# Kernel tuning notes

Measured on AMD Instinct MI355X. Metric: run time of the kernel, lower is better.

Reference implementation:

```python
import jax, jax.numpy as jnp
import numpy as np

F_DIM = 64
GRID_CYL = (512, 48)   # (grid0=azimuth, grid1=z)
CYL_RANGE = (-3.14159265, -2.0, 3.14159265, 4.0)
CYL_VS = ((CYL_RANGE[2] - CYL_RANGE[0]) / GRID_CYL[0], (CYL_RANGE[3] - CYL_RANGE[1]) / GRID_CYL[1])
PC_RANGE = (0.0, -40.0, -3.0, 70.4, 40.0, 1.0)
BEV_VS = (0.32, 0.32)
GRID_BEV = (220, 250)  # (grid0=x, grid1=y)
BEV_SCALE_XY = GRID_BEV[0] * GRID_BEV[1]
BEV_SCALE_Y = GRID_BEV[1]
CYL_SCALE_XY = GRID_CYL[0] * GRID_CYL[1]
CYL_SCALE_Y = GRID_CYL[1]
BN_EPS = 1e-3


def _bn_relu(x, g, b):
    # train-mode BatchNorm1d over point axis; x: [N, C]
    m = x.mean(0)
    v = jnp.mean((x - m) ** 2, 0)
    return jax.nn.relu((x - m) * jax.lax.rsqrt(v + BN_EPS) * g + b)


def setup_inputs():
    rng = np.random.default_rng(0)
    B, NP = 4, 50000
    N = B * NP
    bidx = np.repeat(np.arange(B), NP).astype(np.float32)
    x = rng.uniform(0.5, 70.0, N).astype(np.float32)
    y = rng.uniform(-39.9, 39.9, N).astype(np.float32)
    z = rng.uniform(-2.9, 0.9, N).astype(np.float32)
    inten = rng.uniform(0.0, 1.0, N).astype(np.float32)
    points = np.stack([bidx, x, y, z, inten], 1)
    rho = np.sqrt(x * x + y * y)
    phi = np.arctan2(y, x)
    points_cyl = np.stack([phi, z, rho], 1).astype(np.float32)
    cyl_idxs = np.stack([(phi - CYL_RANGE[0]) / CYL_VS[0], (z - CYL_RANGE[1]) / CYL_VS[1]], 1)
    cyl_idxs = np.minimum(np.maximum(cyl_idxs, 0.0), np.array(GRID_CYL) - 1e-3).astype(np.float32)
    bev_idxs = np.stack([(x - PC_RANGE[0]) / BEV_VS[0], (y - PC_RANGE[1]) / BEV_VS[1]], 1)
    bev_idxs = np.minimum(np.maximum(bev_idxs, 0.0), np.array(GRID_BEV) - 1e-3).astype(np.float32)
    bev_merge = bidx.astype(np.int64) * BEV_SCALE_XY + np.floor(bev_idxs[:, 0]).astype(np.int64) * BEV_SCALE_Y + np.floor(bev_idxs[:, 1]).astype(np.int64)
    bev_unq, bev_inv = np.unique(bev_merge, return_inverse=True)
    cyl_merge = bidx.astype(np.int64) * CYL_SCALE_XY + np.floor(cyl_idxs[:, 0]).astype(np.int64) * CYL_SCALE_Y + np.floor(cyl_idxs[:, 1]).astype(np.int64)
    cyl_unq, cyl_inv = np.unique(cyl_merge, return_inverse=True)

    def lin(o, i):
        return (rng.standard_normal((o, i)) / np.sqrt(i)).astype(np.float32)

    w1 = lin(F_DIM, 16)
    w2 = lin(2 * F_DIM, F_DIM)
    w3 = lin(F_DIM, 2 * F_DIM)
    wc = (rng.standard_normal((F_DIM, F_DIM, 3, 3)) / np.sqrt(F_DIM * 9)).astype(np.float32)

    def bn(c):
        return (1.0 + 0.1 * rng.standard_normal(c)).astype(np.float32), (0.1 * rng.standard_normal(c)).astype(np.float32)

    g1, b1 = bn(F_DIM)
    g2, b2 = bn(2 * F_DIM)
    gc, bc = bn(F_DIM)
    g3, b3 = bn(F_DIM)
    return {
        'points': jnp.asarray(points), 'points_cyl': jnp.asarray(points_cyl),
        'cyl_idxs': jnp.asarray(cyl_idxs), 'bev_idxs': jnp.asarray(bev_idxs),
        'w1': jnp.asarray(w1), 'g1': jnp.asarray(g1), 'b1': jnp.asarray(b1),
        'w2': jnp.asarray(w2), 'g2': jnp.asarray(g2), 'b2': jnp.asarray(b2),
        'wc': jnp.asarray(wc), 'gc': jnp.asarray(gc), 'bc': jnp.asarray(bc),
        'w3': jnp.asarray(w3), 'g3': jnp.asarray(g3), 'b3': jnp.asarray(b3),
        'bev_unq_inv': jnp.asarray(bev_inv.astype(np.int32)),
        'bev_unq_coords': jnp.asarray(bev_unq.astype(np.int32)),
        'cyl_unq_inv': jnp.asarray(cyl_inv.astype(np.int32)),
        'cyl_unq_coords': jnp.asarray(cyl_unq.astype(np.int32)),
        'batch_size': B,
    }


def reference(points, points_cyl, cyl_idxs, bev_idxs, w1, g1, b1, w2, g2, b2, wc, gc, bc, w3, g3, b3, bev_unq_inv, bev_unq_coords, cyl_unq_inv, cyl_unq_coords, batch_size):
    N = points.shape[0]
    xyz = points[:, 1:4]
    feat = points[:, 4:]
    pbatch = points[:, 0].astype(jnp.int32)
    bev_c = jnp.floor(bev_idxs)
    cyl_c = jnp.floor(cyl_idxs)
    Nb = bev_unq_coords.shape[0]
    Nc = cyl_unq_coords.shape[0]
    ones = jnp.ones((N,), points.dtype)
    # scatter_mean + gather centering / clustering features
    cnt_b = jax.ops.segment_sum(ones, bev_unq_inv, Nb)
    bev_mean = jax.ops.segment_sum(xyz, bev_unq_inv, Nb) / cnt_b[:, None]
    bev_f_cluster = (xyz - bev_mean[bev_unq_inv])[:, :2]
    bev_f_center = xyz[:, :2] - ((bev_c + 0.5) * jnp.array(BEV_VS, points.dtype) + jnp.array(PC_RANGE[:2], points.dtype))
    cnt_c = jax.ops.segment_sum(ones, cyl_unq_inv, Nc)
    cyl_mean = jax.ops.segment_sum(points_cyl, cyl_unq_inv, Nc) / cnt_c[:, None]
    cyl_f_cluster = (points_cyl - cyl_mean[cyl_unq_inv])[:, :2]
    cyl_f_center = points_cyl[:, :2] - ((cyl_c + 0.5) * jnp.array(CYL_VS, points.dtype) + jnp.array(CYL_RANGE[:2], points.dtype))
    dist = jnp.sqrt(jnp.sum(xyz ** 2, 1, keepdims=True))
    mvf_in = jnp.concatenate([xyz, points_cyl, bev_f_center, cyl_f_center, bev_f_cluster, cyl_f_cluster, dist, feat], 1)  # [N,16]
    # input_transform: two 1x1 Conv1d (= matmul) + BN + ReLU
    h = _bn_relu(mvf_in @ w1.T, g1, b1)   # [N,64]
    h2 = _bn_relu(h @ w2.T, g2, b2)       # [N,128]
    pt_fea_cyl, pointwise = h2[:, :F_DIM], h2[:, F_DIM:]
    # cyl scatter_max -> dense range-view grid
    cyl_max = jax.ops.segment_max(pt_fea_cyl, cyl_unq_inv, Nc)  # [Nc,64]
    cb = cyl_unq_coords // CYL_SCALE_XY
    rem = cyl_unq_coords % CYL_SCALE_XY
    cx = rem // CYL_SCALE_Y
    cy = rem % CYL_SCALE_Y
    dense = jnp.zeros((batch_size, CYL_SCALE_XY, F_DIM), cyl_max.dtype)
    dense = dense.at[cb, cy * GRID_CYL[0] + cx].set(cyl_max)
    img = dense.reshape(batch_size, GRID_CYL[1], GRID_CYL[0], F_DIM).transpose(0, 3, 2, 1)  # NCHW, H=grid0, W=grid1
    # cyl_net proxy: Conv2d 3x3 + BN + ReLU
    img = jax.lax.conv_general_dilated(img, wc, (1, 1), 'SAME', dimension_numbers=('NCHW', 'OIHW', 'NCHW'))
    m = img.mean((0, 2, 3), keepdims=True)
    v = jnp.mean((img - m) ** 2, (0, 2, 3), keepdims=True)
    img = jax.nn.relu((img - m) * jax.lax.rsqrt(v + BN_EPS) * gc[None, :, None, None] + bc[None, :, None, None])
    im = img.transpose(0, 2, 3, 1)  # [B, grid0, grid1, F]
    # bilinear interpolation of per-point cyl features
    yq, xq = cyl_idxs[:, 0], cyl_idxs[:, 1]
    x0 = jnp.clip(jnp.floor(xq).astype(jnp.int32), 0, GRID_CYL[1] - 1)
    x1 = jnp.clip(jnp.floor(xq).astype(jnp.int32) + 1, 0, GRID_CYL[1] - 1)
    y0 = jnp.clip(jnp.floor(yq).astype(jnp.int32), 0, GRID_CYL[0] - 1)
    y1 = jnp.clip(jnp.floor(yq).astype(jnp.int32) + 1, 0, GRID_CYL[0] - 1)
    Ia = im[pbatch, y0, x0]
    Ib = im[pbatch, y1, x0]
    Ic = im[pbatch, y0, x1]
    Id = im[pbatch, y1, x1]
    x0f, x1f = x0.astype(xq.dtype), x1.astype(xq.dtype)
    y0f, y1f = y0.astype(yq.dtype), y1.astype(yq.dtype)
    wa = (x1f - xq) * (y1f - yq)
    wb_ = (x1f - xq) * (yq - y0f)
    wc_ = (xq - x0f) * (y1f - yq)
    wd = (xq - x0f) * (yq - y0f)
    point_cyl = Ia * wa[:, None] + Ib * wb_[:, None] + Ic * wc_[:, None] + Id * wd[:, None]  # [N,64]
    # mvf pointnet + bev scatter_max
    mvf2 = jnp.concatenate([pointwise, point_cyl], 1)  # [N,128]
    mvf_fea = _bn_relu(mvf2 @ w3.T, g3, b3)            # [N,64]
    bev_max = jax.ops.segment_max(mvf_fea, bev_unq_inv, Nb)  # [Nb,64] pillar features
    vb = bev_unq_coords // BEV_SCALE_XY
    vx = (bev_unq_coords % BEV_SCALE_XY) // BEV_SCALE_Y
    vy = bev_unq_coords % BEV_SCALE_Y
    voxel_coords = jnp.stack([vb, jnp.zeros_like(vb), vy, vx], 1)
    return mvf_fea, bev_max, voxel_coords
```

## Files before the change

kernel.cpp:

```cpp
#include <hip/hip_runtime.h>
#include <math.h>

#define BN_EPS 1e-3f

static constexpr float CR0 = -3.14159265f;
static constexpr float CR1 = -2.0f;
static constexpr float CVS0 = (float)((3.14159265 * 2.0) / 512.0);
static constexpr float CVS1 = (float)(6.0 / 48.0);
#define BEV_SXY (220 * 250)
#define BEV_SY 250

typedef __attribute__((ext_vector_type(8))) __bf16 bf16x8_t;
typedef __attribute__((ext_vector_type(4))) float f32x4_t;

union ABu { uint4 q; unsigned short us[8]; bf16x8_t bf; };

__device__ __forceinline__ float bnr(float x, float a, float b) {
    float v = fmaf(x, a, b);
    return v > 0.f ? v : 0.f;
}
__device__ __forceinline__ float bf2f(unsigned short u) {
    return __uint_as_float(((unsigned)u) << 16);
}
__device__ __forceinline__ unsigned short f2bf(float f) {
    unsigned u = __float_as_uint(f);
    u += 0x7FFFu + ((u >> 16) & 1u);
    return (unsigned short)(u >> 16);
}
__device__ __forceinline__ void bn_ab(const float* st, const float* g, const float* b,
                                      int C, int ch, float invn, float& a, float& bb) {
    float m = st[ch] * invn;
    float var = st[C + ch] * invn - m * m;
    a = g[ch] * rsqrtf(var + BN_EPS);
    bb = b[ch] - m * a;
}

__device__ __forceinline__ unsigned fkey(float f) {
    unsigned u = __float_as_uint(f);
    return (u & 0x80000000u) ? ~u : (u | 0x80000000u);
}
__device__ __forceinline__ float dec_key(unsigned k, float a, float b) {
    if (k == 0u) return 0.f;
    unsigned u = (k & 0x80000000u) ? (k ^ 0x80000000u) : ~k;
    float v = fmaf(__uint_as_float(u), a, b);
    return v > 0.f ? v : 0.f;
}

__global__ void k_scatter_sums(const float* __restrict__ pts, const float* __restrict__ pcyl,
                               const int* __restrict__ binv, const int* __restrict__ cinv,
                               const float* __restrict__ wc, unsigned short* __restrict__ wctb,
                               unsigned long long* __restrict__ bacc,
                               unsigned long long* __restrict__ cacc,
                               int N, int Nb, int Nc) {
    int p = blockIdx.x * blockDim.x + threadIdx.x;
    if (p < 9 * 4096) {
        int j = p & 7, oc = (p >> 3) & 63, quad = (p >> 9) & 3, kc = (p >> 11) & 1, tap = p >> 12;
        int ic = kc * 32 + quad * 8 + j;
        wctb[p] = f2bf(wc[((oc * 64 + ic) * 3 + tap / 3) * 3 + tap % 3]);
    }
    if (p >= N) return;
    float x = pts[p * 5 + 1], y = pts[p * 5 + 2];
    float ph = pcyl[p * 3 + 0], z = pcyl[p * 3 + 1];
    int bi = binv[p], ci = cinv[p];
    unsigned long long xa = (1ull << 44) + (unsigned long long)(x * 1048576.0f + 0.5f);
    unsigned long long ya = (unsigned long long)((y + 40.0f) * 16777216.0f + 0.5f);
    unsigned long long pa = (1ull << 44) + (unsigned long long)((ph + 3.14159265f) * 16777216.0f + 0.5f);
    unsigned long long za = (unsigned long long)((z + 3.0f) * 16777216.0f + 0.5f);
    atomicAdd(&bacc[2 * (long)bi], xa);
    atomicAdd(&bacc[2 * (long)bi + 1], ya);
    atomicAdd(&cacc[2 * (long)ci], pa);
    atomicAdd(&cacc[2 * (long)ci + 1], za);
}

__global__ __launch_bounds__(256) void k_feat_gemm1(const float* __restrict__ pts,
        const float* __restrict__ pcyl, const float* __restrict__ cylidx,
        const float* __restrict__ bevidx, const int* __restrict__ binv,
        const int* __restrict__ cinv, const unsigned long long* __restrict__ bacc,
        const unsigned long long* __restrict__ cacc, const float* __restrict__ w1,
        unsigned short* __restrict__ h1b, int N, int Nb, int Nc) {
    __shared__ float w1s[1024];
    __shared__ unsigned int tbuf[32 * 260];
    int t = threadIdx.x;
    for (int i = t; i < 1024; i += 256) w1s[i] = w1[i];
    __syncthreads();
    int p = blockIdx.x * 256 + t;
    int pc = min(p, N - 1);
    float x = pts[pc * 5 + 1], y = pts[pc * 5 + 2], z = pts[pc * 5 + 3], inten = pts[pc * 5 + 4];
    float ph = pcyl[pc * 3 + 0], zc = pcyl[pc * 3 + 1], rho = pcyl[pc * 3 + 2];
    float ci0 = cylidx[pc * 2 + 0], ci1 = cylidx[pc * 2 + 1];
    float bi0 = bevidx[pc * 2 + 0], bi1 = bevidx[pc * 2 + 1];
    float bc0 = floorf(bi0), bc1 = floorf(bi1);
    float cc0 = floorf(ci0), cc1 = floorf(ci1);
    int bv = binv[pc], cv = cinv[pc];
    const unsigned long long MASK44 = (1ull << 44) - 1ull;
    unsigned long long A = bacc[2 * (long)bv], Bq = bacc[2 * (long)bv + 1];
    float bcnt = (float)(A >> 44);
    float rb = 1.0f / bcnt;
    float bmx = (float)(A & MASK44) * (1.0f / 1048576.0f) * rb;
    float bmy = (float)Bq * (1.0f / 16777216.0f) * rb - 40.0f;
    unsigned long long Cq = cacc[2 * (long)cv], Dq = cacc[2 * (long)cv + 1];
    float ccnt = (float)(Cq >> 44);
    float rc = 1.0f / ccnt;
    float cmp = (float)(Cq & MASK44) * (1.0f / 16777216.0f) * rc - 3.14159265f;
    float cmz = (float)Dq * (1.0f / 16777216.0f) * rc - 3.0f;
    float f[16];
    f[0] = x; f[1] = y; f[2] = z;
    f[3] = ph; f[4] = zc; f[5] = rho;
    f[6] = x - ((bc0 + 0.5f) * 0.32f + 0.0f);
    f[7] = y - ((bc1 + 0.5f) * 0.32f + (-40.0f));
    f[8] = ph - ((cc0 + 0.5f) * CVS0 + CR0);
    f[9] = zc - ((cc1 + 0.5f) * CVS1 + CR1);
    f[10] = x - bmx; f[11] = y - bmy;
    f[12] = ph - cmp; f[13] = zc - cmz;
    f[14] = sqrtf(x * x + y * y + z * z);
    f[15] = inten;
    for (int c2 = 0; c2 < 32; c2++) {
        float s0 = 0.f, s1 = 0.f;
        const float* w0 = &w1s[(2 * c2) * 16];
        const float* w1p = &w1s[(2 * c2 + 1) * 16];
#pragma unroll
        for (int k = 0; k < 16; k++) {
            s0 = fmaf(f[k], w0[k], s0);
            s1 = fmaf(f[k], w1p[k], s1);
        }
        tbuf[c2 * 260 + t] = (unsigned)f2bf(s0) | ((unsigned)f2bf(s1) << 16);
    }
    __syncthreads();
#pragma unroll
    for (int r = 0; r < 4; r++) {
        int cid = t + 256 * r;
        int pp = cid >> 2;
        int gp = blockIdx.x * 256 + pp;
        if (gp < N) {
            int c2b = (cid & 3) * 8;
            uint4 A2, Bv;
            A2.x = tbuf[(c2b + 0) * 260 + pp];
            A2.y = tbuf[(c2b + 1) * 260 + pp];
            A2.z = tbuf[(c2b + 2) * 260 + pp];
            A2.w = tbuf[(c2b + 3) * 260 + pp];
            Bv.x = tbuf[(c2b + 4) * 260 + pp];
            Bv.y = tbuf[(c2b + 5) * 260 + pp];
            Bv.z = tbuf[(c2b + 6) * 260 + pp];
            Bv.w = tbuf[(c2b + 7) * 260 + pp];
            uint4* dst = (uint4*)(h1b + (long)gp * 64 + (cid & 3) * 16);
            dst[0] = A2;
            dst[1] = Bv;
        }
    }
}

__global__ __launch_bounds__(256) void k_stats_v(const unsigned short* __restrict__ buf,
        long T, int C, float* __restrict__ out) {
    int t = threadIdx.x;
    long base = ((long)blockIdx.x * 256 + t) * 8;
    long stride = (long)gridDim.x * 2048;
    float s[8], q[8];
#pragma unroll
    for (int j = 0; j < 8; j++) { s[j] = 0.f; q[j] = 0.f; }
    for (long i = base; i < T; i += stride) {
        ABu u;
        u.q = *(const uint4*)(buf + i);
#pragma unroll
        for (int j = 0; j < 8; j++) {
            float v = bf2f(u.us[j]);
            s[j] += v;
            q[j] = fmaf(v, v, q[j]);
        }
    }
    __shared__ float ls[2048], lq[2048];
#pragma unroll
    for (int j = 0; j < 8; j++) { ls[t * 8 + j] = s[j]; lq[t * 8 + j] = q[j]; }
    __syncthreads();
    if (t < C) {
        int g = t >> 3, j = t & 7;
        int step = C >> 3;
        float ss = 0.f, qq = 0.f;
        for (int tid = g; tid < 256; tid += step) {
            ss += ls[tid * 8 + j];
            qq += lq[tid * 8 + j];
        }
        atomicAdd(&out[t], ss);
        atomicAdd(&out[C + t], qq);
    }
}

__global__ __launch_bounds__(256, 2) void k_gemm2_mfma(const unsigned short* __restrict__ h1b,
        const float* __restrict__ w2, const float* __restrict__ st1,
        const float* __restrict__ g1, const float* __restrict__ b1g, float invn,
        const float* __restrict__ pts, const float* __restrict__ cylidx,
        const float* __restrict__ g2full, unsigned int* __restrict__ gridk,
        unsigned short* __restrict__ h2b, int N) {
    int lane = threadIdx.x & 63;
    int c = lane & 15, quad = lane >> 4;
    int wid = (blockIdx.x * 256 + threadIdx.x) >> 6;
    int nw = gridDim.x * 4;
    bf16x8_t Bf[8][2];
#pragma unroll
    for (int tt = 0; tt < 8; tt++)
#pragma unroll
        for (int kc = 0; kc < 2; kc++) {
            const float* wr = w2 + (tt * 16 + c) * 64 + kc * 32 + quad * 8;
            float4 w0 = *(const float4*)wr;
            float4 w1 = *(const float4*)(wr + 4);
            ABu tmp;
            tmp.us[0] = f2bf(w0.x); tmp.us[1] = f2bf(w0.y);
            tmp.us[2] = f2bf(w0.z); tmp.us[3] = f2bf(w0.w);
            tmp.us[4] = f2bf(w1.x); tmp.us[5] = f2bf(w1.y);
            tmp.us[6] = f2bf(w1.z); tmp.us[7] = f2bf(w1.w);
            Bf[tt][kc] = tmp.bf;
        }
    float a1[16], b1[16];
#pragma unroll
    for (int kc = 0; kc < 2; kc++)
#pragma unroll
        for (int j = 0; j < 8; j++) {
            int ch = kc * 32 + quad * 8 + j;
            bn_ab(st1, g1, b1g, 64, ch, invn, a1[kc * 8 + j], b1[kc * 8 + j]);
        }
    unsigned sx[4];
#pragma unroll
    for (int tt = 0; tt < 4; tt++)
        sx[tt] = (g2full[tt * 16 + c] < 0.f) ? 0x80000000u : 0u;
    int ntiles = (N + 15) >> 4;
    for (int tile = wid; tile < ntiles; tile += nw) {
        int p0 = tile * 16;
        int pa = min(p0 + c, N - 1);
        int bsc = (int)pts[pa * 5];
        int ccx = (int)floorf(cylidx[pa * 2]);
        int ccy = (int)floorf(cylidx[pa * 2 + 1]);
        int cellbase = (((bsc * 512 + ccx) * 48) + ccy) * 64;
        bf16x8_t Af[2];
#pragma unroll
        for (int kc = 0; kc < 2; kc++) {
            ABu u;
            u.q = *(const uint4*)(h1b + (long)pa * 64 + kc * 32 + quad * 8);
            ABu o;
#pragma unroll
            for (int j = 0; j < 8; j++)
                o.us[j] = f2bf(bnr(bf2f(u.us[j]), a1[kc * 8 + j], b1[kc * 8 + j]));
            Af[kc] = o.bf;
        }
        f32x4_t acc[8];
#pragma unroll
        for (int tt = 0; tt < 8; tt++) acc[tt] = (f32x4_t){0.f, 0.f, 0.f, 0.f};
#pragma unroll
        for (int tt = 0; tt < 8; tt++) {
            acc[tt] = __builtin_amdgcn_mfma_f32_16x16x32_bf16(Af[0], Bf[tt][0], acc[tt], 0, 0, 0);
            acc[tt] = __builtin_amdgcn_mfma_f32_16x16x32_bf16(Af[1], Bf[tt][1], acc[tt], 0, 0, 0);
        }
#pragma unroll
        for (int r = 0; r < 4; r++) {
            int cb_r = __shfl(cellbase, quad * 4 + r);
            int pr = p0 + quad * 4 + r;
            bool ok = pr < N;
#pragma unroll
            for (int tt = 0; tt < 8; tt++) {
                unsigned short hv = f2bf(acc[tt][r]);
                if (ok) {
                    h2b[(long)pr * 128 + tt * 16 + c] = hv;
                    if (tt < 4) {
                        float xr = bf2f(hv);
                        unsigned key = fkey(__uint_as_float(__float_as_uint(xr) ^ sx[tt]));
                        atomicMax(&gridk[cb_r + tt * 16 + c], key);
                    }
                }
            }
        }
    }
}

__global__ __launch_bounds__(768) void k_conv_lds(const unsigned int* __restrict__ gridk,
        const unsigned short* __restrict__ wctb, unsigned short* __restrict__ cb,
        const float* __restrict__ st2, const float* __restrict__ g2,
        const float* __restrict__ b2g, float invn) {
    __shared__ unsigned short in_s[4 * 50 * 64];
    __shared__ unsigned short ob_s[2 * 48 * 64];
    __shared__ float as_[64], bs_[64];
    int t = threadIdx.x;
    int lane = t & 63, wv = t >> 6;
    int n = lane & 15, quad = lane >> 4;
    int seg = wv >> 2, tt = wv & 3;
    int blk = blockIdx.x;
    int b = blk >> 8, r0 = (blk & 255) * 2;
    if (t < 64) {
        float av, bv;
        bn_ab(st2, g2, b2g, 128, t, invn, av, bv);
        as_[t] = fabsf(av);
        bs_[t] = bv;
    }
    bf16x8_t Bf[9][2];
    const unsigned short* wb = wctb + quad * 512 + (tt * 16 + n) * 8;
#pragma unroll
    for (int tap = 0; tap < 9; tap++)
#pragma unroll
        for (int kc = 0; kc < 2; kc++) {
            ABu u;
            u.q = *(const uint4*)(wb + (tap * 2 + kc) * 2048);
            Bf[tap][kc] = u.bf;
        }
    __syncthreads();
    for (int c = t; c < 1600; c += 768) {
        int row4 = c / 400;
        int rem = c % 400;
        int px = rem >> 3, ch8 = rem & 7;
        int gr = r0 + row4 - 1, gw = px - 1;
        ABu o;
        if (gr >= 0 && gr < 512 && gw >= 0 && gw < 48) {
            const unsigned int* src = gridk + (((long)b * 512 + gr) * 48 + gw) * 64 + ch8 * 8;
            uint4 k0 = *(const uint4*)src;
            uint4 k1 = *(const uint4*)(src + 4);
            const float* ap = &as_[ch8 * 8];
            const float* bp = &bs_[ch8 * 8];
            o.us[0] = f2bf(dec_key(k0.x, ap[0], bp[0]));
            o.us[1] = f2bf(dec_key(k0.y, ap[1], bp[1]));
            o.us[2] = f2bf(dec_key(k0.z, ap[2], bp[2]));
            o.us[3] = f2bf(dec_key(k0.w, ap[3], bp[3]));
            o.us[4] = f2bf(dec_key(k1.x, ap[4], bp[4]));
            o.us[5] = f2bf(dec_key(k1.y, ap[5], bp[5]));
            o.us[6] = f2bf(dec_key(k1.z, ap[6], bp[6]));
            o.us[7] = f2bf(dec_key(k1.w, ap[7], bp[7]));
        } else {
            o.q = make_uint4(0, 0, 0, 0);
        }
        *(uint4*)&in_s[(row4 * 50 + px) * 64 + ((ch8 ^ (px & 7)) << 3)] = o.q;
    }
    __syncthreads();
    for (int rr = 0; rr < 2; rr++) {
        f32x4_t acc0 = (f32x4_t){0.f, 0.f, 0.f, 0.f};
        f32x4_t acc1 = (f32x4_t){0.f, 0.f, 0.f, 0.f};
#pragma unroll
        for (int tap = 0; tap < 9; tap++) {
            int row4 = tap / 3 + rr;
            int lpx = seg * 16 + n + tap % 3;
            const unsigned short* base = &in_s[(row4 * 50 + lpx) * 64];
            ABu a0, a1;
            a0.q = *(const uint4*)(base + ((quad ^ (lpx & 7)) << 3));
            a1.q = *(const uint4*)(base + (((4 + quad) ^ (lpx & 7)) << 3));
            acc0 = __builtin_amdgcn_mfma_f32_16x16x32_bf16(a0.bf, Bf[tap][0], acc0, 0, 0, 0);
            acc1 = __builtin_amdgcn_mfma_f32_16x16x32_bf16(a1.bf, Bf[tap][1], acc1, 0, 0, 0);
        }
#pragma unroll
        for (int r2 = 0; r2 < 4; r2++) {
            int px = seg * 16 + quad * 4 + r2;
            ob_s[(rr * 48 + px) * 64 + tt * 16 + n] = f2bf(acc0[r2] + acc1[r2]);
        }
    }
    __syncthreads();
    unsigned short* dst = cb + ((long)b * 512 + r0) * 48 * 64;
    *(uint4*)(dst + t * 8) = *(const uint4*)(ob_s + t * 8);
}

__global__ __launch_bounds__(256, 2) void k_gather3_mfma(const unsigned short* __restrict__ h2b,
        const unsigned short* __restrict__ convb, const float* __restrict__ st2,
        const float* __restrict__ g2, const float* __restrict__ b2g,
        const float* __restrict__ stC, const float* __restrict__ gc,
        const float* __restrict__ bcg, float invn, float invnC,
        const float* __restrict__ cylidx, const float* __restrict__ pts,
        const float* __restrict__ w3, unsigned short* __restrict__ h3b, int N) {
    int lane = threadIdx.x & 63;
    int c = lane & 15, quad = lane >> 4;
    int wid = (blockIdx.x * 256 + threadIdx.x) >> 6;
    int nw = gridDim.x * 4;
    bf16x8_t Bf[4][4];
#pragma unroll
    for (int tt = 0; tt < 4; tt++)
#pragma unroll
        for (int kc = 0; kc < 4; kc++) {
            const float* wr = w3 + (tt * 16 + c) * 128 + kc * 32 + quad * 8;
            float4 w0 = *(const float4*)wr;
            float4 w1 = *(const float4*)(wr + 4);
            ABu tmp;
            tmp.us[0] = f2bf(w0.x); tmp.us[1] = f2bf(w0.y);
            tmp.us[2] = f2bf(w0.z); tmp.us[3] = f2bf(w0.w);
            tmp.us[4] = f2bf(w1.x); tmp.us[5] = f2bf(w1.y);
            tmp.us[6] = f2bf(w1.z); tmp.us[7] = f2bf(w1.w);
            Bf[tt][kc] = tmp.bf;
        }
    float a2[16], b2[16], aC[16], bC[16];
#pragma unroll
    for (int kc = 0; kc < 2; kc++)
#pragma unroll
        for (int j = 0; j < 8; j++) {
            int kk = kc * 32 + quad * 8 + j;
            bn_ab(st2, g2, b2g, 128, 64 + kk, invn, a2[kc * 8 + j], b2[kc * 8 + j]);
            bn_ab(stC, gc, bcg, 64, kk, invnC, aC[kc * 8 + j], bC[kc * 8 + j]);
        }
    int ntiles = (N + 15) >> 4;
    for (int tile = wid; tile < ntiles; tile += nw) {
        int p0 = tile * 16;
        int p = min(p0 + c, N - 1);
        float yq = cylidx[p * 2], xq = cylidx[p * 2 + 1];
        int b = (int)pts[p * 5];
        int xf = (int)floorf(xq), yf = (int)floorf(yq);
        int x0 = min(max(xf, 0), 47);
        int x1 = min(max(xf + 1, 0), 47);
        int y0 = min(max(yf, 0), 511);
        int y1 = min(max(yf + 1, 0), 511);
        float x0f = (float)x0, x1f = (float)x1, y0f = (float)y0, y1f = (float)y1;
        float wa = (x1f - xq) * (y1f - yq);
        float wb = (x1f - xq) * (yq - y0f);
        float wc2 = (xq - x0f) * (y1f - yq);
        float wd = (xq - x0f) * (yq - y0f);
        const unsigned short* Ia = convb + (((long)b * 512 + y0) * 48 + x0) * 64;
        const unsigned short* Ib = convb + (((long)b * 512 + y1) * 48 + x0) * 64;
        const unsigned short* Ic = convb + (((long)b * 512 + y0) * 48 + x1) * 64;
        const unsigned short* Id = convb + (((long)b * 512 + y1) * 48 + x1) * 64;
        bf16x8_t Af[4];
#pragma unroll
        for (int kc = 0; kc < 2; kc++) {
            ABu u;
            u.q = *(const uint4*)(h2b + (long)p * 128 + 64 + kc * 32 + quad * 8);
            ABu o;
#pragma unroll
            for (int j = 0; j < 8; j++)
                o.us[j] = f2bf(bnr(bf2f(u.us[j]), a2[kc * 8 + j], b2[kc * 8 + j]));
            Af[kc] = o.bf;
        }
#pragma unroll
        for (int kc = 0; kc < 2; kc++) {
            int cbo = kc * 32 + quad * 8;
            ABu ua, ub, uc, ud;
            ua.q = *(const uint4*)(Ia + cbo);
            ub.q = *(const uint4*)(Ib + cbo);
            uc.q = *(const uint4*)(Ic + cbo);
            ud.q = *(const uint4*)(Id + cbo);
            ABu o;
#pragma unroll
            for (int j = 0; j < 8; j++) {
                float aa = aC[kc * 8 + j], bbv = bC[kc * 8 + j];
                float v = wa * bnr(bf2f(ua.us[j]), aa, bbv) + wb * bnr(bf2f(ub.us[j]), aa, bbv)
                        + wc2 * bnr(bf2f(uc.us[j]), aa, bbv) + wd * bnr(bf2f(ud.us[j]), aa, bbv);
                o.us[j] = f2bf(v);
            }
            Af[2 + kc] = o.bf;
        }
        f32x4_t acc[4];
#pragma unroll
        for (int tt = 0; tt < 4; tt++) acc[tt] = (f32x4_t){0.f, 0.f, 0.f, 0.f};
#pragma unroll
        for (int tt = 0; tt < 4; tt++)
#pragma unroll
            for (int kc = 0; kc < 4; kc++)
                acc[tt] = __builtin_amdgcn_mfma_f32_16x16x32_bf16(Af[kc], Bf[tt][kc], acc[tt], 0, 0, 0);
#pragma unroll
        for (int tt = 0; tt < 4; tt++)
#pragma unroll
            for (int r = 0; r < 4; r++) {
                int pr = p0 + quad * 4 + r;
                if (pr < N) h3b[(long)pr * 64 + tt * 16 + c] = f2bf(acc[tt][r]);
            }
    }
}

__global__ __launch_bounds__(256) void k_out_tile3(const unsigned short* __restrict__ h3b,
        const float* __restrict__ st3, const float* __restrict__ g3,
        const float* __restrict__ b3g, float invn, const int* __restrict__ binv,
        float* __restrict__ out_fea, unsigned int* __restrict__ out_bev,
        const int* __restrict__ bcoords, float* __restrict__ out_vc, int Nb, int N) {
    int t = threadIdx.x, lane = t & 63, w = t >> 6;
    long gid = (long)blockIdx.x * 256 + t;
    if (gid < Nb) {
        int cc = bcoords[gid];
        int vb = cc / BEV_SXY;
        int rem = cc % BEV_SXY;
        int vx = rem / BEV_SY;
        int vy = rem % BEV_SY;
        out_vc[gid * 4 + 0] = (float)vb;
        out_vc[gid * 4 + 1] = 0.f;
        out_vc[gid * 4 + 2] = (float)vy;
        out_vc[gid * 4 + 3] = (float)vx;
    }
    int p = blockIdx.x * 4 + w;
    if (p >= N) return;
    float a, bb;
    bn_ab(st3, g3, b3g, 64, lane, invn, a, bb);
    float v = bnr(bf2f(h3b[(long)p * 64 + lane]), a, bb);
    out_fea[(long)p * 64 + lane] = v;
    int bi = binv[p];
    if (v > 0.f) {
        unsigned uv = __float_as_uint(v);
        unsigned* cell = out_bev + (long)bi * 64;
        unsigned cur = cell[lane];
        if (uv > cur) atomicMax(&cell[lane], uv);
    }
}

extern "C" void kernel_launch(void* const* d_in, const int* in_sizes, int n_in,
                              void* d_out, int out_size, void* d_ws, size_t ws_size,
                              hipStream_t stream) {
    const float* pts = (const float*)d_in[0];
    const float* pcyl = (const float*)d_in[1];
    const float* cylidx = (const float*)d_in[2];
    const float* bevidx = (const float*)d_in[3];
    const float* w1 = (const float*)d_in[4];
    const float* g1 = (const float*)d_in[5];
    const float* b1 = (const float*)d_in[6];
    const float* w2 = (const float*)d_in[7];
    const float* g2 = (const float*)d_in[8];
    const float* b2 = (const float*)d_in[9];
    const float* wc = (const float*)d_in[10];
    const float* gc = (const float*)d_in[11];
    const float* bc = (const float*)d_in[12];
    const float* w3 = (const float*)d_in[13];
    const float* g3 = (const float*)d_in[14];
    const float* b3 = (const float*)d_in[15];
    const int* binv = (const int*)d_in[16];
    const int* bcoords = (const int*)d_in[17];
    const int* cinv = (const int*)d_in[18];
    const int* ccoords = (const int*)d_in[19];
    int N = in_sizes[0] / 5;
    int Nb = in_sizes[17];
    int Nc = in_sizes[19];
    const int B = 4;
    const long GRIDSZ = (long)B * 512 * 48 * 64;
    float invN = 1.0f / (float)N;
    float invC = 1.0f / (float)(B * 512 * 48);

    char* wsb = (char*)d_ws;
    unsigned short* wctb = (unsigned short*)wsb;
    unsigned short* h2b = (unsigned short*)(wsb + 73728);
    unsigned short* h13b = (unsigned short*)(wsb + 73728 + 256L * N);
    unsigned int* gridk = (unsigned int*)(wsb + 73728 + 384L * N);
    unsigned short* convb = (unsigned short*)(gridk + GRIDSZ);
    unsigned long long* bacc = (unsigned long long*)(convb + GRIDSZ);
    unsigned long long* cacc = bacc + 2L * Nb;
    float* stats = (float*)(cacc + 2L * Nc);
    float* st1 = stats, *st2 = stats + 128, *st3 = stats + 384, *stC = stats + 512;

    float* out_fea = (float*)d_out;
    unsigned int* out_bev = (unsigned int*)((float*)d_out + (long)N * 64);
    float* out_vc = (float*)d_out + (long)N * 64 + (long)Nb * 64;

    hipMemsetAsync(gridk, 0, (size_t)GRIDSZ * 4, stream);
    hipMemsetAsync(bacc, 0, (size_t)((2L * Nb + 2L * Nc) * 8 + 768 * 4), stream);
    hipMemsetAsync(out_bev, 0, (size_t)Nb * 64 * 4, stream);

    int nb256 = (N + 255) / 256;
    k_scatter_sums<<<nb256, 256, 0, stream>>>(pts, pcyl, binv, cinv, wc, wctb, bacc, cacc, N, Nb, Nc);
    k_feat_gemm1<<<nb256, 256, 0, stream>>>(pts, pcyl, cylidx, bevidx, binv, cinv, bacc, cacc, w1, h13b, N, Nb, Nc);
    k_stats_v<<<512, 256, 0, stream>>>(h13b, 64L * N, 64, st1);
    k_gemm2_mfma<<<512, 256, 0, stream>>>(h13b, w2, st1, g1, b1, invN, pts, cylidx, g2, gridk, h2b, N);
    k_stats_v<<<512, 256, 0, stream>>>(h2b, 128L * N, 128, st2);
    k_conv_lds<<<1024, 768, 0, stream>>>(gridk, wctb, convb, st2, g2, b2, invN);
    k_stats_v<<<512, 256, 0, stream>>>(convb, GRIDSZ, 64, stC);
    k_gather3_mfma<<<512, 256, 0, stream>>>(h2b, convb, st2, g2, b2, stC, gc, bc, invN, invC, cylidx, pts, w3, h13b, N);
    k_stats_v<<<512, 256, 0, stream>>>(h13b, 64L * N, 64, st3);
    k_out_tile3<<<(N + 3) / 4, 256, 0, stream>>>(h13b, st3, g3, b3, invN, binv, out_fea, out_bev, bcoords, out_vc, Nb, N);
}
```

Before: 444.1 us.

## Fuse BatchNorm statistics into producer kernels and halve the h2 buffer

Removes the four standalone k_stats_v passes. Each producer kernel (gemm1, gemm2, conv, gather3) now accumulates per-channel sum and sum-of-squares of its bf16 outputs in registers or LDS, reduces across the wave, and adds them atomically into the stats buffer. gemm2 no longer writes the first 64 channels of h2 to memory, since they only feed the grid atomicMax, so h2 becomes 64 channels wide and gather3 reads it that way. Grid sizes for gemm2 and gather3 are doubled. The cost is more float atomics on the stats arrays and a non-deterministic summation order.

```diff
diff --git a/kernel.cpp b/kernel.cpp
--- a/kernel.cpp
+++ b/kernel.cpp
@@ -77,7 +77,8 @@
         const float* __restrict__ bevidx, const int* __restrict__ binv,
         const int* __restrict__ cinv, const unsigned long long* __restrict__ bacc,
         const unsigned long long* __restrict__ cacc, const float* __restrict__ w1,
-        unsigned short* __restrict__ h1b, int N, int Nb, int Nc) {
+        unsigned short* __restrict__ h1b, float* __restrict__ st1o,
+        int N, int Nb, int Nc) {
     __shared__ float w1s[1024];
     __shared__ unsigned int tbuf[32 * 260];
     int t = threadIdx.x;
@@ -147,40 +148,30 @@
             dst[1] = Bv;
         }
     }
-}
-
-__global__ __launch_bounds__(256) void k_stats_v(const unsigned short* __restrict__ buf,
-        long T, int C, float* __restrict__ out) {
-    int t = threadIdx.x;
-    long base = ((long)blockIdx.x * 256 + t) * 8;
-    long stride = (long)gridDim.x * 2048;
-    float s[8], q[8];
-#pragma unroll
-    for (int j = 0; j < 8; j++) { s[j] = 0.f; q[j] = 0.f; }
-    for (long i = base; i < T; i += stride) {
-        ABu u;
-        u.q = *(const uint4*)(buf + i);
-#pragma unroll
-        for (int j = 0; j < 8; j++) {
-            float v = bf2f(u.us[j]);
-            s[j] += v;
-            q[j] = fmaf(v, v, q[j]);
-        }
-    }
-    __shared__ float ls[2048], lq[2048];
-#pragma unroll
-    for (int j = 0; j < 8; j++) { ls[t * 8 + j] = s[j]; lq[t * 8 + j] = q[j]; }
-    __syncthreads();
-    if (t < C) {
-        int g = t >> 3, j = t & 7;
-        int step = C >> 3;
+    {
+        int ch = t & 63, grp = t >> 6;
+        int c2 = ch >> 1, sh = (ch & 1) << 4;
+        int nval = min(256, N - blockIdx.x * 256);
         float ss = 0.f, qq = 0.f;
-        for (int tid = g; tid < 256; tid += step) {
-            ss += ls[tid * 8 + j];
-            qq += lq[tid * 8 + j];
-        }
-        atomicAdd(&out[t], ss);
-        atomicAdd(&out[C + t], qq);
+        for (int i = 0; i < 64; i++) {
+            int pp = grp * 64 + i;
+            if (pp < nval) {
+                unsigned uw = tbuf[c2 * 260 + pp];
+                float v = bf2f((unsigned short)(uw >> sh));
+                ss += v;
+                qq = fmaf(v, v, qq);
+            }
+        }
+        __syncthreads();
+        w1s[t] = ss;
+        w1s[256 + t] = qq;
+        __syncthreads();
+        if (t < 64) {
+            float S = w1s[t] + w1s[64 + t] + w1s[128 + t] + w1s[192 + t];
+            float Q = w1s[256 + t] + w1s[320 + t] + w1s[384 + t] + w1s[448 + t];
+            atomicAdd(&st1o[t], S);
+            atomicAdd(&st1o[64 + t], Q);
+        }
     }
 }
 
@@ -189,7 +180,7 @@
         const float* __restrict__ g1, const float* __restrict__ b1g, float invn,
         const float* __restrict__ pts, const float* __restrict__ cylidx,
         const float* __restrict__ g2full, unsigned int* __restrict__ gridk,
-        unsigned short* __restrict__ h2b, int N) {
+        unsigned short* __restrict__ h2b, float* __restrict__ st2o, int N) {
     int lane = threadIdx.x & 63;
     int c = lane & 15, quad = lane >> 4;
     int wid = (blockIdx.x * 256 + threadIdx.x) >> 6;
@@ -221,6 +212,9 @@
 #pragma unroll
     for (int tt = 0; tt < 4; tt++)
         sx[tt] = (g2full[tt * 16 + c] < 0.f) ? 0x80000000u : 0u;
+    float s8[8], q8[8];
+#pragma unroll
+    for (int tt = 0; tt < 8; tt++) { s8[tt] = 0.f; q8[tt] = 0.f; }
     int ntiles = (N + 15) >> 4;
     for (int tile = wid; tile < ntiles; tile += nw) {
         int p0 = tile * 16;
@@ -257,22 +251,35 @@
             for (int tt = 0; tt < 8; tt++) {
                 unsigned short hv = f2bf(acc[tt][r]);
                 if (ok) {
-                    h2b[(long)pr * 128 + tt * 16 + c] = hv;
+                    float xr = bf2f(hv);
+                    s8[tt] += xr;
+                    q8[tt] = fmaf(xr, xr, q8[tt]);
                     if (tt < 4) {
-                        float xr = bf2f(hv);
                         unsigned key = fkey(__uint_as_float(__float_as_uint(xr) ^ sx[tt]));
                         atomicMax(&gridk[cb_r + tt * 16 + c], key);
+                    } else {
+                        h2b[(long)pr * 64 + (tt - 4) * 16 + c] = hv;
                     }
                 }
             }
         }
     }
+#pragma unroll
+    for (int tt = 0; tt < 8; tt++) {
+        float ss = s8[tt], qq = q8[tt];
+        ss += __shfl_xor(ss, 16); ss += __shfl_xor(ss, 32);
+        qq += __shfl_xor(qq, 16); qq += __shfl_xor(qq, 32);
+        if (quad == 0) {
+            atomicAdd(&st2o[tt * 16 + c], ss);
+            atomicAdd(&st2o[128 + tt * 16 + c], qq);
+        }
+    }
 }
 
 __global__ __launch_bounds__(768) void k_conv_lds(const unsigned int* __restrict__ gridk,
         const unsigned short* __restrict__ wctb, unsigned short* __restrict__ cb,
         const float* __restrict__ st2, const float* __restrict__ g2,
-        const float* __restrict__ b2g, float invn) {
+        const float* __restrict__ b2g, float invn, float* __restrict__ stCo) {
     __shared__ unsigned short in_s[4 * 50 * 64];
     __shared__ unsigned short ob_s[2 * 48 * 64];
     __shared__ float as_[64], bs_[64];
@@ -325,6 +332,7 @@
         *(uint4*)&in_s[(row4 * 50 + px) * 64 + ((ch8 ^ (px & 7)) << 3)] = o.q;
     }
     __syncthreads();
+    float sC = 0.f, qC = 0.f;
     for (int rr = 0; rr < 2; rr++) {
         f32x4_t acc0 = (f32x4_t){0.f, 0.f, 0.f, 0.f};
         f32x4_t acc1 = (f32x4_t){0.f, 0.f, 0.f, 0.f};
@@ -342,8 +350,18 @@
 #pragma unroll
         for (int r2 = 0; r2 < 4; r2++) {
             int px = seg * 16 + quad * 4 + r2;
-            ob_s[(rr * 48 + px) * 64 + tt * 16 + n] = f2bf(acc0[r2] + acc1[r2]);
-        }
+            unsigned short hv = f2bf(acc0[r2] + acc1[r2]);
+            ob_s[(rr * 48 + px) * 64 + tt * 16 + n] = hv;
+            float xr = bf2f(hv);
+            sC += xr;
+            qC = fmaf(xr, xr, qC);
+        }
+    }
+    sC += __shfl_xor(sC, 16); sC += __shfl_xor(sC, 32);
+    qC += __shfl_xor(qC, 16); qC += __shfl_xor(qC, 32);
+    if (quad == 0) {
+        atomicAdd(&stCo[tt * 16 + n], sC);
+        atomicAdd(&stCo[64 + tt * 16 + n], qC);
     }
     __syncthreads();
     unsigned short* dst = cb + ((long)b * 512 + r0) * 48 * 64;
@@ -356,7 +374,8 @@
         const float* __restrict__ stC, const float* __restrict__ gc,
         const float* __restrict__ bcg, float invn, float invnC,
         const float* __restrict__ cylidx, const float* __restrict__ pts,
-        const float* __restrict__ w3, unsigned short* __restrict__ h3b, int N) {
+        const float* __restrict__ w3, unsigned short* __restrict__ h3b,
+        float* __restrict__ st3o, int N) {
     int lane = threadIdx.x & 63;
     int c = lane & 15, quad = lane >> 4;
     int wid = (blockIdx.x * 256 + threadIdx.x) >> 6;
@@ -385,6 +404,9 @@
             bn_ab(st2, g2, b2g, 128, 64 + kk, invn, a2[kc * 8 + j], b2[kc * 8 + j]);
             bn_ab(stC, gc, bcg, 64, kk, invnC, aC[kc * 8 + j], bC[kc * 8 + j]);
         }
+    float s4[4], q4[4];
+#pragma unroll
+    for (int tt = 0; tt < 4; tt++) { s4[tt] = 0.f; q4[tt] = 0.f; }
     int ntiles = (N + 15) >> 4;
     for (int tile = wid; tile < ntiles; tile += nw) {
         int p0 = tile * 16;
@@ -409,7 +431,7 @@
 #pragma unroll
         for (int kc = 0; kc < 2; kc++) {
             ABu u;
-            u.q = *(const uint4*)(h2b + (long)p * 128 + 64 + kc * 32 + quad * 8);
+            u.q = *(const uint4*)(h2b + (long)p * 64 + kc * 32 + quad * 8);
             ABu o;
 #pragma unroll
             for (int j = 0; j < 8; j++)
@@ -447,8 +469,24 @@
 #pragma unroll
             for (int r = 0; r < 4; r++) {
                 int pr = p0 + quad * 4 + r;
-                if (pr < N) h3b[(long)pr * 64 + tt * 16 + c] = f2bf(acc[tt][r]);
+                if (pr < N) {
+                    unsigned short hv = f2bf(acc[tt][r]);
+                    h3b[(long)pr * 64 + tt * 16 + c] = hv;
+                    float xr = bf2f(hv);
+                    s4[tt] += xr;
+                    q4[tt] = fmaf(xr, xr, q4[tt]);
+                }
             }
+    }
+#pragma unroll
+    for (int tt = 0; tt < 4; tt++) {
+        float ss = s4[tt], qq = q4[tt];
+        ss += __shfl_xor(ss, 16); ss += __shfl_xor(ss, 32);
+        qq += __shfl_xor(qq, 16); qq += __shfl_xor(qq, 32);
+        if (quad == 0) {
+            atomicAdd(&st3o[tt * 16 + c], ss);
+            atomicAdd(&st3o[64 + tt * 16 + c], qq);
+        }
     }
 }
 
@@ -519,8 +557,8 @@
     char* wsb = (char*)d_ws;
     unsigned short* wctb = (unsigned short*)wsb;
     unsigned short* h2b = (unsigned short*)(wsb + 73728);
-    unsigned short* h13b = (unsigned short*)(wsb + 73728 + 256L * N);
-    unsigned int* gridk = (unsigned int*)(wsb + 73728 + 384L * N);
+    unsigned short* h13b = (unsigned short*)(wsb + 73728 + 128L * N);
+    unsigned int* gridk = (unsigned int*)(wsb + 73728 + 256L * N);
     unsigned short* convb = (unsigned short*)(gridk + GRIDSZ);
     unsigned long long* bacc = (unsigned long long*)(convb + GRIDSZ);
     unsigned long long* cacc = bacc + 2L * Nb;
@@ -537,13 +575,9 @@
 
     int nb256 = (N + 255) / 256;
     k_scatter_sums<<<nb256, 256, 0, stream>>>(pts, pcyl, binv, cinv, wc, wctb, bacc, cacc, N, Nb, Nc);
-    k_feat_gemm1<<<nb256, 256, 0, stream>>>(pts, pcyl, cylidx, bevidx, binv, cinv, bacc, cacc, w1, h13b, N, Nb, Nc);
-    k_stats_v<<<512, 256, 0, stream>>>(h13b, 64L * N, 64, st1);
-    k_gemm2_mfma<<<512, 256, 0, stream>>>(h13b, w2, st1, g1, b1, invN, pts, cylidx, g2, gridk, h2b, N);
-    k_stats_v<<<512, 256, 0, stream>>>(h2b, 128L * N, 128, st2);
-    k_conv_lds<<<1024, 768, 0, stream>>>(gridk, wctb, convb, st2, g2, b2, invN);
-    k_stats_v<<<512, 256, 0, stream>>>(convb, GRIDSZ, 64, stC);
-    k_gather3_mfma<<<512, 256, 0, stream>>>(h2b, convb, st2, g2, b2, stC, gc, bc, invN, invC, cylidx, pts, w3, h13b, N);
-    k_stats_v<<<512, 256, 0, stream>>>(h13b, 64L * N, 64, st3);
+    k_feat_gemm1<<<nb256, 256, 0, stream>>>(pts, pcyl, cylidx, bevidx, binv, cinv, bacc, cacc, w1, h13b, st1, N, Nb, Nc);
+    k_gemm2_mfma<<<1024, 256, 0, stream>>>(h13b, w2, st1, g1, b1, invN, pts, cylidx, g2, gridk, h2b, st2, N);
+    k_conv_lds<<<1024, 768, 0, stream>>>(gridk, wctb, convb, st2, g2, b2, invN, stC);
+    k_gather3_mfma<<<1024, 256, 0, stream>>>(h2b, convb, st2, g2, b2, stC, gc, bc, invN, invC, cylidx, pts, w3, h13b, st3, N);
     k_out_tile3<<<(N + 3) / 4, 256, 0, stream>>>(h13b, st3, g3, b3, invN, binv, out_fea, out_bev, bcoords, out_vc, Nb, N);
 }
```

Measured after the change: 879.0 us. +97.9%, slower.
